# Kernel tuning notes

Measured on AMD Instinct MI355X. Metric: run time of the kernel, lower is better.

Reference implementation:

```python
import jax, jax.numpy as jnp
import numpy as np

# Bamba-9B-like mamba mixer config
HID = 2048           # hidden_size
I = 4096             # intermediate_size = mamba_expand * hidden_size
H = 64               # mamba_n_heads
P = 64               # mamba_d_head  (H*P == I)
N = 128              # mamba_d_state
G = 1                # mamba_n_groups
K = 4                # mamba_d_conv
CHUNK = 256          # mamba_chunk_size
EPS = 1e-5
CONV_DIM = I + 2 * G * N          # 4352
PROJ = I + CONV_DIM + H           # 8512


def setup_inputs() -> dict:
    key = jax.random.key(0)
    ks = jax.random.split(key, 4)
    bsz, seq = 1, 2048
    x = jax.random.normal(ks[0], (bsz, seq, HID), jnp.float32)
    W_in = jax.random.normal(ks[1], (PROJ, HID), jnp.float32) * 0.02
    conv_w = jax.random.normal(ks[2], (CONV_DIM, K), jnp.float32) * 0.2
    conv_b = jnp.zeros((CONV_DIM,), jnp.float32)
    dt_bias = jnp.ones((H,), jnp.float32)
    A_log = jnp.log(jnp.arange(1, H + 1, dtype=jnp.float32))
    D = jnp.ones((H,), jnp.float32)
    norm_w = jnp.ones((I,), jnp.float32)
    W_out = jax.random.normal(ks[3], (HID, I), jnp.float32) * 0.02
    return dict(x=x, W_in=W_in, conv_w=conv_w, conv_b=conv_b, dt_bias=dt_bias,
                A_log=A_log, D=D, norm_w=norm_w, W_out=W_out)


def causal_conv1d_silu(u, w, b):
    # u: [b,s,d] depthwise causal conv, kernel K, then SiLU
    bsz, s, d = u.shape
    up = jnp.pad(u, ((0, 0), (K - 1, 0), (0, 0)))
    acc = jnp.zeros_like(u)
    for k in range(K):  # K=4, fixed small loop
        acc = acc + up[:, k:k + s, :] * w[:, k]
    return jax.nn.silu(acc + b)


def ssd_chunked(xh, dt, A, Bm, Cm, Dp):
    # Exact mamba_chunk_scan_combined math (dt already softplus'd):
    #   h_t = exp(dt_t * A) h_{t-1} + dt_t * B_t x_t^T ;  y_t = C_t . h_t + D x_t
    # xh [b,s,h,p], dt [b,s,h], A [h], Bm/Cm [b,s,g,n], Dp [h]
    b, s, h, p = xh.shape
    n = Bm.shape[-1]
    nc = s // CHUNK
    rep = h // G
    xr = xh.reshape(b, nc, CHUNK, h, p)
    dtr = dt.reshape(b, nc, CHUNK, h)
    Bh = jnp.repeat(Bm.reshape(b, nc, CHUNK, G, n), rep, axis=3)  # [b,c,l,h,n]
    Ch = jnp.repeat(Cm.reshape(b, nc, CHUNK, G, n), rep, axis=3)
    dA = dtr * A                      # [b,c,l,h]
    Acum = jnp.cumsum(dA, axis=2)     # [b,c,l,h]
    # intra-chunk causal part
    mask = jnp.tril(jnp.ones((CHUNK, CHUNK), bool))
    L = jnp.where(mask[None, None, :, :, None],
                  jnp.exp(Acum[:, :, :, None, :] - Acum[:, :, None, :, :]), 0.0)
    CB = jnp.einsum('bcthn,bcshn->bctsh', Ch, Bh)
    Y = jnp.einsum('bctsh,bcsh,bcshp->bcthp', CB * L, dtr, xr)
    # per-chunk end states and inter-chunk recurrence
    dte = jnp.exp(Acum[:, :, -1:, :] - Acum) * dtr            # decay-to-end * dt
    states = jnp.einsum('bclh,bclhn,bclhp->bchpn', dte, Bh, xr)
    cdecay = jnp.exp(Acum[:, :, -1, :])                       # [b,c,h]

    def step(carry, inp):
        st, dec = inp  # st [b,h,p,n], dec [b,h]
        return carry * dec[:, :, None, None] + st, carry      # emit state at chunk start

    init = jnp.zeros((b, h, p, n), xh.dtype)
    _, prev = jax.lax.scan(step, init,
                           (jnp.moveaxis(states, 1, 0), jnp.moveaxis(cdecay, 1, 0)))
    prev = jnp.moveaxis(prev, 0, 1)                           # [b,c,h,p,n]
    Y = Y + jnp.einsum('bclhn,bclh,bchpn->bclhp', Ch, jnp.exp(Acum), prev)
    Y = Y + xr * Dp[None, None, None, :, None]                # D skip
    return Y.reshape(b, s, h * p)


def reference(x, W_in, conv_w, conv_b, dt_bias, A_log, D, norm_w, W_out):
    bsz, s, _ = x.shape
    proj = jnp.einsum('bsd,pd->bsp', x, W_in)
    gate, hbc, dt_raw = jnp.split(proj, [I, I + CONV_DIM], axis=-1)
    hbc = causal_conv1d_silu(hbc, conv_w, conv_b)
    xs, Bm, Cm = jnp.split(hbc, [I, I + G * N], axis=-1)
    dt = jax.nn.softplus(dt_raw + dt_bias)                    # dt_softplus + dt_bias
    A = -jnp.exp(A_log)
    y = ssd_chunked(xs.reshape(bsz, s, H, P), dt, A,
                    Bm.reshape(bsz, s, G, N), Cm.reshape(bsz, s, G, N), D)
    # gated RMSNorm (gate applied before normalization, norm_before_gate=False)
    y = y * jax.nn.silu(gate)
    var = jnp.mean(y * y, axis=-1, keepdims=True)
    y = y * jax.lax.rsqrt(var + EPS) * norm_w
    return jnp.einsum('bsi,di->bsd', y, W_out)
```

## Files before the change

kernel.cpp:

```cpp
#include <hip/hip_runtime.h>
#include <math.h>

static constexpr int kS     = 2048;
static constexpr int kHID   = 2048;
static constexpr int kI     = 4096;
static constexpr int kH     = 64;
static constexpr int kP     = 64;
static constexpr int kN     = 128;
static constexpr int kConv  = 4352;
static constexpr int kProj  = 8512;
static constexpr int kChunk = 256;
static constexpr int kNC    = 8;
static constexpr float kEps = 1e-5f;

typedef __attribute__((ext_vector_type(8))) short short8;
typedef __attribute__((ext_vector_type(4))) float floatx4;

__device__ __forceinline__ float4 f4fma(float a, float4 b, float4 c) {
    c.x += a * b.x; c.y += a * b.y; c.z += a * b.z; c.w += a * b.w; return c;
}
__device__ __forceinline__ float siluf(float x) {
    return x / (1.f + __expf(-x));
}
__device__ __forceinline__ unsigned short f2bf(float f) {
    unsigned int u = __float_as_uint(f);
    return (unsigned short)((u + 0x7FFFu + ((u >> 16) & 1u)) >> 16);
}
__device__ __forceinline__ void gll16(const void* g, void* l) {
    __builtin_amdgcn_global_load_lds(
        (const __attribute__((address_space(1))) void*)g,
        (__attribute__((address_space(3))) void*)l, 16, 0, 0);
}

__global__ __launch_bounds__(256)
void cast_bf16_k(const float* __restrict__ in, unsigned short* __restrict__ out)
{
    size_t i = ((size_t)blockIdx.x * 256 + threadIdx.x) * 8;
    float4 a = *(const float4*)&in[i];
    float4 b = *(const float4*)&in[i + 4];
    ushort4 u0 = {f2bf(a.x), f2bf(a.y), f2bf(a.z), f2bf(a.w)};
    ushort4 u1 = {f2bf(b.x), f2bf(b.y), f2bf(b.z), f2bf(b.w)};
    *(ushort4*)&out[i] = u0;
    *(ushort4*)&out[i + 4] = u1;
}

__global__ __launch_bounds__(256)
void gemm_bt_bf16(const unsigned short* __restrict__ A,
                  const unsigned short* __restrict__ B,
                  float* __restrict__ C, int M, int N, int K)
{
    __shared__ unsigned short As[128 * 64];
    __shared__ unsigned short Bs[128 * 64];
    const int tid = threadIdx.x;
    const int lane = tid & 63, quad = lane >> 4, l15 = lane & 15;
    const int wave = tid >> 6;

    const int Nt = (N + 127) >> 7;
    const int mainN = Nt & ~7;
    int bi = blockIdx.x, mt, nt;
    if (bi < mainN * 16) {
        nt = ((bi >> 7) << 3) | (bi & 7);
        mt = (bi >> 3) & 15;
    } else {
        int r = bi - mainN * 16, rem = Nt - mainN;
        nt = mainN + r % rem; mt = r / rem;
    }
    const int m0 = mt * 128, n0 = nt * 128;
    const int wm = (wave & 1) * 64, wn = (wave >> 1) * 64;

    floatx4 acc[4][4] = {};

    int rowS[4], lcS[4];
#pragma unroll
    for (int i = 0; i < 4; ++i) {
        int f = tid + 256 * i;
        rowS[i] = f >> 3;
        lcS[i] = ((f & 7) ^ (rowS[i] & 7)) * 8;
    }

    for (int k0 = 0; k0 < K; k0 += 64) {
#pragma unroll
        for (int i = 0; i < 4; ++i) {
            int ra = m0 + rowS[i];
            gll16(&A[(size_t)ra * K + k0 + lcS[i]], &As[(size_t)(tid + 256 * i) * 8]);
        }
#pragma unroll
        for (int i = 0; i < 4; ++i) {
            int rb = n0 + rowS[i]; if (rb > N - 1) rb = N - 1;
            gll16(&B[(size_t)rb * K + k0 + lcS[i]], &Bs[(size_t)(tid + 256 * i) * 8]);
        }
        __syncthreads();

        short8 af[4][2], bf[4][2];
#pragma unroll
        for (int ks = 0; ks < 2; ++ks) {
            const int ph = ((ks * 4 + quad) ^ (l15 & 7)) * 8;
#pragma unroll
            for (int mi = 0; mi < 4; ++mi)
                af[mi][ks] = *(const short8*)&As[(size_t)(wm + mi * 16 + l15) * 64 + ph];
#pragma unroll
            for (int ni = 0; ni < 4; ++ni)
                bf[ni][ks] = *(const short8*)&Bs[(size_t)(wn + ni * 16 + l15) * 64 + ph];
        }
#pragma unroll
        for (int ks = 0; ks < 2; ++ks)
#pragma unroll
            for (int mi = 0; mi < 4; ++mi)
#pragma unroll
                for (int ni = 0; ni < 4; ++ni)
                    acc[mi][ni] = __builtin_amdgcn_mfma_f32_16x16x32_bf16(
                        af[mi][ks], bf[ni][ks], acc[mi][ni], 0, 0, 0);
        __syncthreads();
    }

#pragma unroll
    for (int mi = 0; mi < 4; ++mi)
#pragma unroll
        for (int ni = 0; ni < 4; ++ni) {
            int col = n0 + wn + ni * 16 + l15;
            if (col < N) {
#pragma unroll
                for (int r = 0; r < 4; ++r) {
                    int row = m0 + wm + mi * 16 + quad * 4 + r;
                    C[(size_t)row * N + col] = acc[mi][ni][r];
                }
            }
        }
}

__global__ __launch_bounds__(256)
void conv_silu_k(const float* __restrict__ proj, const float* __restrict__ cw,
                 const float* __restrict__ cb, float* __restrict__ convout)
{
    int idx = blockIdx.x * 256 + threadIdx.x;
    int d = idx % kConv, t = idx / kConv;
    float acc = cb[d];
#pragma unroll
    for (int k = 0; k < 4; ++k) {
        int ts = t + k - 3;
        float u = (ts >= 0) ? proj[(size_t)ts * kProj + kI + d] : 0.f;
        acc += u * cw[d * 4 + k];
    }
    convout[idx] = siluf(acc);
}

__global__ __launch_bounds__(256)
void dt_cumsum_k(const float* __restrict__ proj, const float* __restrict__ dt_bias,
                 const float* __restrict__ A_log, float* __restrict__ dt,
                 float* __restrict__ acum)
{
    __shared__ float wsum[4];
    const int c = blockIdx.x >> 6, h = blockIdx.x & 63;
    const int l = threadIdx.x, t = c * kChunk + l;
    float a = -expf(A_log[h]);
    float z = proj[(size_t)t * kProj + kI + kConv + h] + dt_bias[h];
    float d = (z > 20.f) ? z : log1pf(expf(z));
    dt[t * kH + h] = d;
    float v = d * a;
    int lane = l & 63, w = l >> 6;
#pragma unroll
    for (int off = 1; off < 64; off <<= 1) {
        float u = __shfl_up(v, off);
        if (lane >= off) v += u;
    }
    if (lane == 63) wsum[w] = v;
    __syncthreads();
    float add = 0.f;
    for (int i = 0; i < w; ++i) add += wsum[i];
    acum[t * kH + h] = v + add;
}

__global__ __launch_bounds__(256)
void states_k(const float* __restrict__ conv, const float* __restrict__ dt,
              const float* __restrict__ acum, float* __restrict__ states)
{
    __shared__ float Bl[64][132];
    __shared__ float Xl[64][68];
    __shared__ float Wl[64];
    const int c = blockIdx.x >> 6, h = blockIdx.x & 63;
    const int tid = threadIdx.x;
    const int p = tid & 63, ng = tid >> 6;
    const float aend = acum[(size_t)(c * kChunk + 255) * kH + h];
    float4 acc[8];
#pragma unroll
    for (int i = 0; i < 8; ++i) acc[i] = make_float4(0.f, 0.f, 0.f, 0.f);

    for (int lt = 0; lt < 4; ++lt) {
        int tbase = c * kChunk + lt * 64;
#pragma unroll
        for (int r = 0; r < 8; ++r) {
            int f = tid + 256 * r;
            int ll = f >> 5, c4 = (f & 31) * 4;
            *(float4*)&Bl[ll][c4] =
                *(const float4*)&conv[(size_t)(tbase + ll) * kConv + kI + c4];
        }
#pragma unroll
        for (int r = 0; r < 4; ++r) {
            int f = tid + 256 * r;
            int ll = f >> 4, c4 = (f & 15) * 4;
            *(float4*)&Xl[ll][c4] =
                *(const float4*)&conv[(size_t)(tbase + ll) * kConv + h * kP + c4];
        }
        if (tid < 64) {
            int t = tbase + tid;
            Wl[tid] = __expf(aend - acum[(size_t)t * kH + h]) * dt[(size_t)t * kH + h];
        }
        __syncthreads();
        for (int ll = 0; ll < 64; ++ll) {
            float xv = Xl[ll][p] * Wl[ll];
#pragma unroll
            for (int j = 0; j < 8; ++j) {
                float4 b = *(const float4*)&Bl[ll][ng * 32 + j * 4];
                acc[j] = f4fma(xv, b, acc[j]);
            }
        }
        __syncthreads();
    }
    size_t base = ((size_t)(c * kH + h) * kP + p) * kN + ng * 32;
#pragma unroll
    for (int j = 0; j < 8; ++j) *(float4*)&states[base + j * 4] = acc[j];
}

__global__ __launch_bounds__(256)
void scan_k(const float* __restrict__ states, const float* __restrict__ acum,
            float* __restrict__ prev)
{
    const int h = blockIdx.x >> 3, seg = blockIdx.x & 7;
    const int e = (seg * 256 + threadIdx.x) * 4;
    float4 carry = make_float4(0.f, 0.f, 0.f, 0.f);
    for (int c = 0; c < kNC; ++c) {
        size_t base = (size_t)(c * kH + h) * (kP * kN);
        *(float4*)&prev[base + e] = carry;
        float dec = __expf(acum[(size_t)(c * kChunk + 255) * kH + h]);
        float4 st = *(const float4*)&states[base + e];
        carry.x = carry.x * dec + st.x; carry.y = carry.y * dec + st.y;
        carry.z = carry.z * dec + st.z; carry.w = carry.w * dec + st.w;
    }
}

__global__ __launch_bounds__(256)
void ssd_y3_k(const float* __restrict__ conv, const float* __restrict__ dt,
              const float* __restrict__ acum, const float* __restrict__ prev,
              const float* __restrict__ Dp, float* __restrict__ Y)
{
    __shared__ unsigned short Cb[64 * 136];
    __shared__ unsigned short Bb[64 * 136];
    __shared__ unsigned short Xt[64 * 72];
    __shared__ unsigned short Wb[64 * 72];
    __shared__ float At[64], Asv[64], Dtv[64];

    const int bi = blockIdx.x;
    const int ti = bi & 3, h = (bi >> 2) & 63, c = bi >> 8;
    const int tid = threadIdx.x;
    const int wave = tid >> 6, lane = tid & 63;
    const int quad = lane >> 4, l15 = lane & 15;
    const int trow0 = c * kChunk + ti * 64;
    const float Dh = Dp[h];

#pragma unroll
    for (int r = 0; r < 8; ++r) {
        int f = tid + 256 * r;
        int row = f >> 5, c4 = (f & 31) * 4;
        float4 v = *(const float4*)&conv[(size_t)(trow0 + row) * kConv + kI + kN + c4];
        ushort4 u = {f2bf(v.x), f2bf(v.y), f2bf(v.z), f2bf(v.w)};
        *(ushort4*)&Cb[row * 136 + c4] = u;
    }
    const size_t pbase = (size_t)(c * kH + h) * (kP * kN);
#pragma unroll
    for (int r = 0; r < 8; ++r) {
        int f = tid + 256 * r;
        int row = f >> 5, c4 = (f & 31) * 4;
        float4 v = *(const float4*)&prev[pbase + (size_t)row * kN + c4];
        ushort4 u = {f2bf(v.x), f2bf(v.y), f2bf(v.z), f2bf(v.w)};
        *(ushort4*)&Bb[row * 136 + c4] = u;
    }
    if (tid < 64) At[tid] = acum[(size_t)(trow0 + tid) * kH + h];
    __syncthreads();

    floatx4 yacc[4] = {};
#pragma unroll
    for (int ks = 0; ks < 4; ++ks) {
        short8 a = *(const short8*)&Cb[(wave * 16 + l15) * 136 + ks * 32 + quad * 8];
#pragma unroll
        for (int ni = 0; ni < 4; ++ni) {
            short8 b = *(const short8*)&Bb[(ni * 16 + l15) * 136 + ks * 32 + quad * 8];
            yacc[ni] = __builtin_amdgcn_mfma_f32_16x16x32_bf16(a, b, yacc[ni], 0, 0, 0);
        }
    }
    {
        float eAr[4];
#pragma unroll
        for (int r = 0; r < 4; ++r) eAr[r] = __expf(At[wave * 16 + quad * 4 + r]);
#pragma unroll
        for (int ni = 0; ni < 4; ++ni)
#pragma unroll
            for (int r = 0; r < 4; ++r) yacc[ni][r] *= eAr[r];
    }

    for (int si = 0; si <= ti; ++si) {
        const int srow0 = c * kChunk + si * 64;
        __syncthreads();
#pragma unroll
        for (int r = 0; r < 8; ++r) {
            int f = tid + 256 * r;
            int row = f >> 5, c4 = (f & 31) * 4;
            float4 v = *(const float4*)&conv[(size_t)(srow0 + row) * kConv + kI + c4];
            ushort4 u = {f2bf(v.x), f2bf(v.y), f2bf(v.z), f2bf(v.w)};
            *(ushort4*)&Bb[row * 136 + c4] = u;
        }
#pragma unroll
        for (int it = 0; it < 2; ++it) {
            int f = tid + 256 * it;
            int p = f & 63, sb = (f >> 6) * 8;
            float vs[8];
#pragma unroll
            for (int j = 0; j < 8; ++j)
                vs[j] = conv[(size_t)(srow0 + sb + j) * kConv + h * kP + p];
            ushort4 u0 = {f2bf(vs[0]), f2bf(vs[1]), f2bf(vs[2]), f2bf(vs[3])};
            ushort4 u1 = {f2bf(vs[4]), f2bf(vs[5]), f2bf(vs[6]), f2bf(vs[7])};
            *(ushort4*)&Xt[p * 72 + sb] = u0;
            *(ushort4*)&Xt[p * 72 + sb + 4] = u1;
        }
        if (tid < 64) {
            Asv[tid] = acum[(size_t)(srow0 + tid) * kH + h];
            Dtv[tid] = dt[(size_t)(srow0 + tid) * kH + h];
        }
        __syncthreads();

        floatx4 sacc[4] = {};
#pragma unroll
        for (int ks = 0; ks < 4; ++ks) {
            short8 a = *(const short8*)&Cb[(wave * 16 + l15) * 136 + ks * 32 + quad * 8];
#pragma unroll
            for (int ni = 0; ni < 4; ++ni) {
                short8 b = *(const short8*)&Bb[(ni * 16 + l15) * 136 + ks * 32 + quad * 8];
                sacc[ni] = __builtin_amdgcn_mfma_f32_16x16x32_bf16(a, b, sacc[ni], 0, 0, 0);
            }
        }

        const bool diag = (si == ti);
#pragma unroll
        for (int ni = 0; ni < 4; ++ni) {
            int s_ = ni * 16 + l15;
            float as = Asv[s_], dts = Dtv[s_];
#pragma unroll
            for (int r = 0; r < 4; ++r) {
                int tl = wave * 16 + quad * 4 + r;
                float w = sacc[ni][r] * __expf(At[tl] - as) * dts;
                if (diag) {
                    if (s_ > tl) w = 0.f;
                    else if (s_ == tl) w += Dh;
                }
                Wb[tl * 72 + s_] = f2bf(w);
            }
        }
#pragma unroll
        for (int ks = 0; ks < 2; ++ks) {
            short8 aw = *(const short8*)&Wb[(wave * 16 + l15) * 72 + ks * 32 + quad * 8];
#pragma unroll
            for (int ni = 0; ni < 4; ++ni) {
                short8 xb = *(const short8*)&Xt[(ni * 16 + l15) * 72 + ks * 32 + quad * 8];
                yacc[ni] = __builtin_amdgcn_mfma_f32_16x16x32_bf16(aw, xb, yacc[ni], 0, 0, 0);
            }
        }
    }

#pragma unroll
    for (int ni = 0; ni < 4; ++ni)
#pragma unroll
        for (int r = 0; r < 4; ++r)
            Y[(size_t)(trow0 + wave * 16 + quad * 4 + r) * kI + h * kP + ni * 16 + l15]
                = yacc[ni][r];
}

__global__ __launch_bounds__(256)
void rmsnorm_gate_k(const float* __restrict__ Y, const float* __restrict__ proj,
                    const float* __restrict__ nw, unsigned short* __restrict__ Yb)
{
    __shared__ float red[4];
    const int t = blockIdx.x, tid = threadIdx.x;
    const float* yrow = &Y[(size_t)t * kI];
    const float* grow = &proj[(size_t)t * kProj];
    float v[16];
    float ss = 0.f;
#pragma unroll
    for (int j = 0; j < 4; ++j) {
        int i = (tid + 256 * j) * 4;
        float4 y4 = *(const float4*)&yrow[i];
        float4 g4 = *(const float4*)&grow[i];
        float a = y4.x * siluf(g4.x), bq = y4.y * siluf(g4.y);
        float cq = y4.z * siluf(g4.z), d = y4.w * siluf(g4.w);
        v[j * 4 + 0] = a; v[j * 4 + 1] = bq; v[j * 4 + 2] = cq; v[j * 4 + 3] = d;
        ss += a * a + bq * bq + cq * cq + d * d;
    }
#pragma unroll
    for (int off = 32; off > 0; off >>= 1) ss += __shfl_down(ss, off);
    if ((tid & 63) == 0) red[tid >> 6] = ss;
    __syncthreads();
    float sum = red[0] + red[1] + red[2] + red[3];
    float rr = rsqrtf(sum * (1.f / kI) + kEps);
#pragma unroll
    for (int j = 0; j < 4; ++j) {
        int i = (tid + 256 * j) * 4;
        float4 w4 = *(const float4*)&nw[i];
        ushort4 o;
        o.x = f2bf(v[j * 4 + 0] * rr * w4.x);
        o.y = f2bf(v[j * 4 + 1] * rr * w4.y);
        o.z = f2bf(v[j * 4 + 2] * rr * w4.z);
        o.w = f2bf(v[j * 4 + 3] * rr * w4.w);
        *(ushort4*)&Yb[(size_t)t * kI + i] = o;
    }
}

extern "C" void kernel_launch(void* const* d_in, const int* in_sizes, int n_in,
                              void* d_out, int out_size, void* d_ws, size_t ws_size,
                              hipStream_t stream)
{
    const float* x       = (const float*)d_in[0];
    const float* W_in    = (const float*)d_in[1];
    const float* conv_w  = (const float*)d_in[2];
    const float* conv_b  = (const float*)d_in[3];
    const float* dt_bias = (const float*)d_in[4];
    const float* A_log   = (const float*)d_in[5];
    const float* Dp      = (const float*)d_in[6];
    const float* norm_w  = (const float*)d_in[7];
    const float* W_out   = (const float*)d_in[8];
    float* out = (float*)d_out;

    float* ws   = (float*)d_ws;
    float* proj = ws;
    float* conv = proj + (size_t)kS * kProj;
    float* dtb  = conv + (size_t)kS * kConv;
    float* acum = dtb + (size_t)kS * kH;
    float* R1   = acum + (size_t)kS * kH;
    float* prev   = R1;
    float* Y      = R1 + (size_t)kNC * kH * kP * kN;
    float* states = Y;
    unsigned short* Wb  = (unsigned short*)R1;
    unsigned short* Yb  = (unsigned short*)R1;
    unsigned short* xb  = (unsigned short*)conv;
    unsigned short* Wob = (unsigned short*)conv;

    dim3 blk(256);
    const int NtP = (kProj + 127) / 128;
    const int NtO = kHID / 128;
    cast_bf16_k<<<(kS * kHID) / 2048, blk, 0, stream>>>(x, xb);
    cast_bf16_k<<<(kProj * kHID) / 2048, blk, 0, stream>>>(W_in, Wb);
    gemm_bt_bf16<<<NtP * 16, blk, 0, stream>>>(xb, Wb, proj, kS, kProj, kHID);
    conv_silu_k<<<(kS * kConv) / 256, blk, 0, stream>>>(proj, conv_w, conv_b, conv);
    dt_cumsum_k<<<kNC * kH, blk, 0, stream>>>(proj, dt_bias, A_log, dtb, acum);
    states_k<<<kNC * kH, blk, 0, stream>>>(conv, dtb, acum, states);
    scan_k<<<kH * 8, blk, 0, stream>>>(states, acum, prev);
    ssd_y3_k<<<kNC * kH * 4, blk, 0, stream>>>(conv, dtb, acum, prev, Dp, Y);
    rmsnorm_gate_k<<<kS, blk, 0, stream>>>(Y, proj, norm_w, Yb);
    cast_bf16_k<<<(kHID * kI) / 2048, blk, 0, stream>>>(W_out, Wob);
    gemm_bt_bf16<<<NtO * 16, blk, 0, stream>>>(Yb, Wob, out, kS, kHID, kI);
}
```

Baseline: 523.5 us.

## Emit bf16 transposed conv outputs and use MFMA for chunk states

The conv+SiLU kernel now writes its outputs as bf16 in layouts suited to later stages: a transposed X, B in row-major and transposed forms, and C. The states kernel replaces its scalar fp32 outer-product loop with bf16 MFMA. The y kernel loads its operands with direct global-to-LDS copies into XOR-swizzled shared memory instead of converting fp32 inside the kernel. This removes repeated fp32 loads and conversions and the strided X gathers, at the cost of extra bf16 rounding (X is rounded twice in the states path) and a more involved transpose step in the conv kernel.

Result: faster. 492.1 us (-6.0%).

```diff
diff --git a/kernel.cpp b/kernel.cpp
--- a/kernel.cpp
+++ b/kernel.cpp
@@ -14,17 +14,18 @@
 static constexpr float kEps = 1e-5f;
 
 typedef __attribute__((ext_vector_type(8))) short short8;
+typedef __attribute__((ext_vector_type(8))) unsigned short ushort8v;
 typedef __attribute__((ext_vector_type(4))) float floatx4;
 
-__device__ __forceinline__ float4 f4fma(float a, float4 b, float4 c) {
-    c.x += a * b.x; c.y += a * b.y; c.z += a * b.z; c.w += a * b.w; return c;
-}
 __device__ __forceinline__ float siluf(float x) {
     return x / (1.f + __expf(-x));
 }
 __device__ __forceinline__ unsigned short f2bf(float f) {
     unsigned int u = __float_as_uint(f);
     return (unsigned short)((u + 0x7FFFu + ((u >> 16) & 1u)) >> 16);
+}
+__device__ __forceinline__ float bf2f(unsigned short u) {
+    return __uint_as_float((unsigned int)u << 16);
 }
 __device__ __forceinline__ void gll16(const void* g, void* l) {
     __builtin_amdgcn_global_load_lds(
@@ -129,19 +130,58 @@
 }
 
 __global__ __launch_bounds__(256)
-void conv_silu_k(const float* __restrict__ proj, const float* __restrict__ cw,
-                 const float* __restrict__ cb, float* __restrict__ convout)
-{
-    int idx = blockIdx.x * 256 + threadIdx.x;
-    int d = idx % kConv, t = idx / kConv;
-    float acc = cb[d];
-#pragma unroll
-    for (int k = 0; k < 4; ++k) {
-        int ts = t + k - 3;
-        float u = (ts >= 0) ? proj[(size_t)ts * kProj + kI + d] : 0.f;
-        acc += u * cw[d * 4 + k];
-    }
-    convout[idx] = siluf(acc);
+void conv_silu2_k(const float* __restrict__ proj, const float* __restrict__ cw,
+                  const float* __restrict__ cb,
+                  unsigned short* __restrict__ XT, unsigned short* __restrict__ Bg,
+                  unsigned short* __restrict__ Btg, unsigned short* __restrict__ Cg)
+{
+    __shared__ __attribute__((aligned(16))) unsigned short T[64][264];
+    const int bd = blockIdx.x % 68, bt = blockIdx.x / 68;
+    const int d0 = bd * 64, t0 = bt * 256;
+    const int tid = threadIdx.x;
+    const int dl = tid & 63;
+    const int d = d0 + dl;
+    const float b0 = cb[d];
+    const float w0 = cw[d * 4 + 0], w1 = cw[d * 4 + 1];
+    const float w2 = cw[d * 4 + 2], w3 = cw[d * 4 + 3];
+    for (int it = 0; it < 64; ++it) {
+        int tl = it * 4 + (tid >> 6);
+        int t = t0 + tl;
+        const float* pc = &proj[(size_t)t * kProj + kI + d];
+        float acc = b0 + w3 * pc[0];
+        if (t >= 1) acc += w2 * pc[-(ptrdiff_t)kProj];
+        if (t >= 2) acc += w1 * pc[-(ptrdiff_t)(2 * kProj)];
+        if (t >= 3) acc += w0 * pc[-(ptrdiff_t)(3 * kProj)];
+        T[dl][tl] = f2bf(siluf(acc));
+    }
+    __syncthreads();
+
+    if (d0 < kI) {
+        int row = tid >> 2, cg = (tid & 3) * 64;
+#pragma unroll
+        for (int j = 0; j < 8; ++j)
+            *(ushort8v*)&XT[(size_t)(d0 + row) * kS + t0 + cg + j * 8] =
+                *(const ushort8v*)&T[row][cg + j * 8];
+    } else if (d0 < kI + kN) {
+        int n0 = d0 - kI;
+        int row = tid >> 2, cg = (tid & 3) * 64;
+#pragma unroll
+        for (int j = 0; j < 8; ++j)
+            *(ushort8v*)&Btg[(size_t)(n0 + row) * kS + t0 + cg + j * 8] =
+                *(const ushort8v*)&T[row][cg + j * 8];
+        for (int pass = 0; pass < 16; ++pass) {
+            int tl = pass * 16 + (tid >> 4), nq = (tid & 15) * 4;
+            ushort4 v = {T[nq][tl], T[nq + 1][tl], T[nq + 2][tl], T[nq + 3][tl]};
+            *(ushort4*)&Bg[(size_t)(t0 + tl) * kN + n0 + nq] = v;
+        }
+    } else {
+        int n0 = d0 - (kI + kN);
+        for (int pass = 0; pass < 16; ++pass) {
+            int tl = pass * 16 + (tid >> 4), nq = (tid & 15) * 4;
+            ushort4 v = {T[nq][tl], T[nq + 1][tl], T[nq + 2][tl], T[nq + 3][tl]};
+            *(ushort4*)&Cg[(size_t)(t0 + tl) * kN + n0 + nq] = v;
+        }
+    }
 }
 
 __global__ __launch_bounds__(256)
@@ -171,54 +211,74 @@
 }
 
 __global__ __launch_bounds__(256)
-void states_k(const float* __restrict__ conv, const float* __restrict__ dt,
-              const float* __restrict__ acum, float* __restrict__ states)
-{
-    __shared__ float Bl[64][132];
-    __shared__ float Xl[64][68];
-    __shared__ float Wl[64];
+void states2_k(const unsigned short* __restrict__ XT,
+               const unsigned short* __restrict__ Btg,
+               const float* __restrict__ dt, const float* __restrict__ acum,
+               float* __restrict__ states)
+{
+    __shared__ __attribute__((aligned(16))) unsigned short Aw[64 * 72];
+    __shared__ __attribute__((aligned(16))) unsigned short Bs[128 * 64];
+    __shared__ float Wl[256];
     const int c = blockIdx.x >> 6, h = blockIdx.x & 63;
     const int tid = threadIdx.x;
-    const int p = tid & 63, ng = tid >> 6;
+    const int wave = tid >> 6, lane = tid & 63;
+    const int quad = lane >> 4, l15 = lane & 15;
     const float aend = acum[(size_t)(c * kChunk + 255) * kH + h];
-    float4 acc[8];
-#pragma unroll
-    for (int i = 0; i < 8; ++i) acc[i] = make_float4(0.f, 0.f, 0.f, 0.f);
-
+    {
+        int t = c * kChunk + tid;
+        Wl[tid] = __expf(aend - acum[(size_t)t * kH + h]) * dt[(size_t)t * kH + h];
+    }
+    __syncthreads();
+
+    floatx4 acc[4][2] = {};
     for (int lt = 0; lt < 4; ++lt) {
-        int tbase = c * kChunk + lt * 64;
-#pragma unroll
-        for (int r = 0; r < 8; ++r) {
-            int f = tid + 256 * r;
-            int ll = f >> 5, c4 = (f & 31) * 4;
-            *(float4*)&Bl[ll][c4] =
-                *(const float4*)&conv[(size_t)(tbase + ll) * kConv + kI + c4];
-        }
-#pragma unroll
-        for (int r = 0; r < 4; ++r) {
-            int f = tid + 256 * r;
-            int ll = f >> 4, c4 = (f & 15) * 4;
-            *(float4*)&Xl[ll][c4] =
-                *(const float4*)&conv[(size_t)(tbase + ll) * kConv + h * kP + c4];
-        }
-        if (tid < 64) {
-            int t = tbase + tid;
-            Wl[tid] = __expf(aend - acum[(size_t)t * kH + h]) * dt[(size_t)t * kH + h];
+        const int s0 = c * kChunk + lt * 64;
+#pragma unroll
+        for (int i = 0; i < 2; ++i) {
+            int f = tid + 256 * i;
+            int p = f >> 3, sc = (f & 7) * 8;
+            ushort8v xv = *(const ushort8v*)&XT[(size_t)(h * 64 + p) * kS + s0 + sc];
+            ushort8v o;
+#pragma unroll
+            for (int j = 0; j < 8; ++j)
+                o[j] = f2bf(bf2f(xv[j]) * Wl[lt * 64 + sc + j]);
+            *(ushort8v*)&Aw[p * 72 + sc] = o;
+        }
+#pragma unroll
+        for (int i = 0; i < 4; ++i) {
+            int f = tid + 256 * i;
+            int n = f >> 3, ph = f & 7, lg = ph ^ (n & 7);
+            gll16(&Btg[(size_t)n * kS + s0 + lg * 8], &Bs[(size_t)f * 8]);
         }
         __syncthreads();
-        for (int ll = 0; ll < 64; ++ll) {
-            float xv = Xl[ll][p] * Wl[ll];
-#pragma unroll
-            for (int j = 0; j < 8; ++j) {
-                float4 b = *(const float4*)&Bl[ll][ng * 32 + j * 4];
-                acc[j] = f4fma(xv, b, acc[j]);
+#pragma unroll
+        for (int ks = 0; ks < 2; ++ks) {
+            short8 bfr[2];
+#pragma unroll
+            for (int nj = 0; nj < 2; ++nj) {
+                int n = (wave * 2 + nj) * 16 + l15;
+                int ph = (ks * 4 + quad) ^ (n & 7);
+                bfr[nj] = *(const short8*)&Bs[n * 64 + ph * 8];
             }
+#pragma unroll
+            for (int pi = 0; pi < 4; ++pi) {
+                short8 af = *(const short8*)&Aw[(pi * 16 + l15) * 72 + ks * 32 + quad * 8];
+                acc[pi][0] = __builtin_amdgcn_mfma_f32_16x16x32_bf16(af, bfr[0], acc[pi][0], 0, 0, 0);
+                acc[pi][1] = __builtin_amdgcn_mfma_f32_16x16x32_bf16(af, bfr[1], acc[pi][1], 0, 0, 0);
+            }
         }
         __syncthreads();
     }
-    size_t base = ((size_t)(c * kH + h) * kP + p) * kN + ng * 32;
-#pragma unroll
-    for (int j = 0; j < 8; ++j) *(float4*)&states[base + j * 4] = acc[j];
+    const size_t base = (size_t)(c * kH + h) * (kP * kN);
+#pragma unroll
+    for (int pi = 0; pi < 4; ++pi)
+#pragma unroll
+        for (int nj = 0; nj < 2; ++nj) {
+            int n = (wave * 2 + nj) * 16 + l15;
+#pragma unroll
+            for (int r = 0; r < 4; ++r)
+                states[base + (size_t)(pi * 16 + quad * 4 + r) * kN + n] = acc[pi][nj][r];
+        }
 }
 
 __global__ __launch_bounds__(256)
@@ -239,14 +299,17 @@
 }
 
 __global__ __launch_bounds__(256)
-void ssd_y3_k(const float* __restrict__ conv, const float* __restrict__ dt,
-              const float* __restrict__ acum, const float* __restrict__ prev,
-              const float* __restrict__ Dp, float* __restrict__ Y)
-{
-    __shared__ unsigned short Cb[64 * 136];
-    __shared__ unsigned short Bb[64 * 136];
-    __shared__ unsigned short Xt[64 * 72];
-    __shared__ unsigned short Wb[64 * 72];
+void ssd_y4_k(const unsigned short* __restrict__ Cg,
+              const unsigned short* __restrict__ Bg,
+              const unsigned short* __restrict__ XT,
+              const float* __restrict__ dt, const float* __restrict__ acum,
+              const float* __restrict__ prev, const float* __restrict__ Dp,
+              float* __restrict__ Y)
+{
+    __shared__ __attribute__((aligned(16))) unsigned short Cb[64 * 128];
+    __shared__ __attribute__((aligned(16))) unsigned short Bb[64 * 128];
+    __shared__ __attribute__((aligned(16))) unsigned short Xt[64 * 64];
+    __shared__ __attribute__((aligned(16))) unsigned short Wb[64 * 72];
     __shared__ float At[64], Asv[64], Dtv[64];
 
     const int bi = blockIdx.x;
@@ -258,12 +321,10 @@
     const float Dh = Dp[h];
 
 #pragma unroll
-    for (int r = 0; r < 8; ++r) {
-        int f = tid + 256 * r;
-        int row = f >> 5, c4 = (f & 31) * 4;
-        float4 v = *(const float4*)&conv[(size_t)(trow0 + row) * kConv + kI + kN + c4];
-        ushort4 u = {f2bf(v.x), f2bf(v.y), f2bf(v.z), f2bf(v.w)};
-        *(ushort4*)&Cb[row * 136 + c4] = u;
+    for (int i = 0; i < 4; ++i) {
+        int f = tid + 256 * i;
+        int row = f >> 4, ph = f & 15, lg = ph ^ (row & 15);
+        gll16(&Cg[(size_t)(trow0 + row) * kN + lg * 8], &Cb[(size_t)f * 8]);
     }
     const size_t pbase = (size_t)(c * kH + h) * (kP * kN);
 #pragma unroll
@@ -272,7 +333,8 @@
         int row = f >> 5, c4 = (f & 31) * 4;
         float4 v = *(const float4*)&prev[pbase + (size_t)row * kN + c4];
         ushort4 u = {f2bf(v.x), f2bf(v.y), f2bf(v.z), f2bf(v.w)};
-        *(ushort4*)&Bb[row * 136 + c4] = u;
+        int dst = row * 128 + ((((f & 31) >> 1) ^ (row & 15)) * 8) + (f & 1) * 4;
+        *(ushort4*)&Bb[dst] = u;
     }
     if (tid < 64) At[tid] = acum[(size_t)(trow0 + tid) * kH + h];
     __syncthreads();
@@ -280,10 +342,11 @@
     floatx4 yacc[4] = {};
 #pragma unroll
     for (int ks = 0; ks < 4; ++ks) {
-        short8 a = *(const short8*)&Cb[(wave * 16 + l15) * 136 + ks * 32 + quad * 8];
+        int cha = (ks * 4 + quad) ^ l15;
+        short8 a = *(const short8*)&Cb[(wave * 16 + l15) * 128 + cha * 8];
 #pragma unroll
         for (int ni = 0; ni < 4; ++ni) {
-            short8 b = *(const short8*)&Bb[(ni * 16 + l15) * 136 + ks * 32 + quad * 8];
+            short8 b = *(const short8*)&Bb[(ni * 16 + l15) * 128 + cha * 8];
             yacc[ni] = __builtin_amdgcn_mfma_f32_16x16x32_bf16(a, b, yacc[ni], 0, 0, 0);
         }
     }
@@ -301,25 +364,16 @@
         const int srow0 = c * kChunk + si * 64;
         __syncthreads();
 #pragma unroll
-        for (int r = 0; r < 8; ++r) {
-            int f = tid + 256 * r;
-            int row = f >> 5, c4 = (f & 31) * 4;
-            float4 v = *(const float4*)&conv[(size_t)(srow0 + row) * kConv + kI + c4];
-            ushort4 u = {f2bf(v.x), f2bf(v.y), f2bf(v.z), f2bf(v.w)};
-            *(ushort4*)&Bb[row * 136 + c4] = u;
-        }
-#pragma unroll
-        for (int it = 0; it < 2; ++it) {
-            int f = tid + 256 * it;
-            int p = f & 63, sb = (f >> 6) * 8;
-            float vs[8];
-#pragma unroll
-            for (int j = 0; j < 8; ++j)
-                vs[j] = conv[(size_t)(srow0 + sb + j) * kConv + h * kP + p];
-            ushort4 u0 = {f2bf(vs[0]), f2bf(vs[1]), f2bf(vs[2]), f2bf(vs[3])};
-            ushort4 u1 = {f2bf(vs[4]), f2bf(vs[5]), f2bf(vs[6]), f2bf(vs[7])};
-            *(ushort4*)&Xt[p * 72 + sb] = u0;
-            *(ushort4*)&Xt[p * 72 + sb + 4] = u1;
+        for (int i = 0; i < 4; ++i) {
+            int f = tid + 256 * i;
+            int row = f >> 4, ph = f & 15, lg = ph ^ (row & 15);
+            gll16(&Bg[(size_t)(srow0 + row) * kN + lg * 8], &Bb[(size_t)f * 8]);
+        }
+#pragma unroll
+        for (int i = 0; i < 2; ++i) {
+            int f = tid + 256 * i;
+            int p = f >> 3, ph = f & 7, lg = ph ^ (p & 7);
+            gll16(&XT[(size_t)(h * 64 + p) * kS + srow0 + lg * 8], &Xt[(size_t)f * 8]);
         }
         if (tid < 64) {
             Asv[tid] = acum[(size_t)(srow0 + tid) * kH + h];
@@ -330,10 +384,11 @@
         floatx4 sacc[4] = {};
 #pragma unroll
         for (int ks = 0; ks < 4; ++ks) {
-            short8 a = *(const short8*)&Cb[(wave * 16 + l15) * 136 + ks * 32 + quad * 8];
+            int cha = (ks * 4 + quad) ^ l15;
+            short8 a = *(const short8*)&Cb[(wave * 16 + l15) * 128 + cha * 8];
 #pragma unroll
             for (int ni = 0; ni < 4; ++ni) {
-                short8 b = *(const short8*)&Bb[(ni * 16 + l15) * 136 + ks * 32 + quad * 8];
+                short8 b = *(const short8*)&Bb[(ni * 16 + l15) * 128 + cha * 8];
                 sacc[ni] = __builtin_amdgcn_mfma_f32_16x16x32_bf16(a, b, sacc[ni], 0, 0, 0);
             }
         }
@@ -359,7 +414,8 @@
             short8 aw = *(const short8*)&Wb[(wave * 16 + l15) * 72 + ks * 32 + quad * 8];
 #pragma unroll
             for (int ni = 0; ni < 4; ++ni) {
-                short8 xb = *(const short8*)&Xt[(ni * 16 + l15) * 72 + ks * 32 + quad * 8];
+                int ph = ((ks * 4 + quad) ^ (l15 & 7)) * 8;
+                short8 xb = *(const short8*)&Xt[(ni * 16 + l15) * 64 + ph];
                 yacc[ni] = __builtin_amdgcn_mfma_f32_16x16x32_bf16(aw, xb, yacc[ni], 0, 0, 0);
             }
         }
@@ -429,17 +485,19 @@
 
     float* ws   = (float*)d_ws;
     float* proj = ws;
-    float* conv = proj + (size_t)kS * kProj;
-    float* dtb  = conv + (size_t)kS * kConv;
+    unsigned short* XT  = (unsigned short*)(proj + (size_t)kS * kProj);
+    unsigned short* Bg  = XT + (size_t)kI * kS;
+    unsigned short* Btg = Bg + (size_t)kS * kN;
+    unsigned short* Cg  = Btg + (size_t)kN * kS;
+    float* dtb  = (float*)(Cg + (size_t)kS * kN);
     float* acum = dtb + (size_t)kS * kH;
-    float* R1   = acum + (size_t)kS * kH;
-    float* prev   = R1;
-    float* Y      = R1 + (size_t)kNC * kH * kP * kN;
+    float* prev = acum + (size_t)kS * kH;
+    float* Y    = prev + (size_t)kNC * kH * kP * kN;
     float* states = Y;
-    unsigned short* Wb  = (unsigned short*)R1;
-    unsigned short* Yb  = (unsigned short*)R1;
-    unsigned short* xb  = (unsigned short*)conv;
-    unsigned short* Wob = (unsigned short*)conv;
+    unsigned short* xb  = XT;
+    unsigned short* Wb  = (unsigned short*)prev;
+    unsigned short* Yb  = (unsigned short*)prev;
+    unsigned short* Wob = XT;
 
     dim3 blk(256);
     const int NtP = (kProj + 127) / 128;
@@ -447,11 +505,11 @@
     cast_bf16_k<<<(kS * kHID) / 2048, blk, 0, stream>>>(x, xb);
     cast_bf16_k<<<(kProj * kHID) / 2048, blk, 0, stream>>>(W_in, Wb);
     gemm_bt_bf16<<<NtP * 16, blk, 0, stream>>>(xb, Wb, proj, kS, kProj, kHID);
-    conv_silu_k<<<(kS * kConv) / 256, blk, 0, stream>>>(proj, conv_w, conv_b, conv);
+    conv_silu2_k<<<68 * 8, blk, 0, stream>>>(proj, conv_w, conv_b, XT, Bg, Btg, Cg);
     dt_cumsum_k<<<kNC * kH, blk, 0, stream>>>(proj, dt_bias, A_log, dtb, acum);
-    states_k<<<kNC * kH, blk, 0, stream>>>(conv, dtb, acum, states);
+    states2_k<<<kNC * kH, blk, 0, stream>>>(XT, Btg, dtb, acum, states);
     scan_k<<<kH * 8, blk, 0, stream>>>(states, acum, prev);
-    ssd_y3_k<<<kNC * kH * 4, blk, 0, stream>>>(conv, dtb, acum, prev, Dp, Y);
+    ssd_y4_k<<<kNC * kH * 4, blk, 0, stream>>>(Cg, Bg, XT, dtb, acum, prev, Dp, Y);
     rmsnorm_gate_k<<<kS, blk, 0, stream>>>(Y, proj, norm_w, Yb);
     cast_bf16_k<<<(kHID * kI) / 2048, blk, 0, stream>>>(W_out, Wob);
     gemm_bt_bf16<<<NtO * 16, blk, 0, stream>>>(Yb, Wob, out, kS, kHID, kI);
```
